# Kernel tuning notes

Hardware: AMD Instinct MI355X
Metric: run time of the kernel (lower is better)

## Reference

```python
import jax, jax.numpy as jnp
import numpy as np

B, S, H = 2, 2048, 2048
NH = 16
HD = H // NH          # 128
ROT = HD // 4         # rotary_dim = head_dim * 0.25 = 32
VP = 320              # v_proj_dim
BASE = 10000.0


def setup_inputs() -> dict:
    key = jax.random.key(0)
    ks = jax.random.split(key, 10)
    sc = lambda fan_in: 1.0 / np.sqrt(fan_in)
    return {
        "hidden_states": jax.random.normal(ks[0], (B, S, H), jnp.float32),
        "Wqkv": jax.random.normal(ks[1], (3 * H, H), jnp.float32) * sc(H),
        "bqkv": jnp.zeros((3 * H,), jnp.float32),
        "Wc": jax.random.normal(ks[2], (VP, H), jnp.float32) * sc(H),
        "bc": jnp.zeros((VP,), jnp.float32),
        "Wr": jax.random.normal(ks[3], (H, VP), jnp.float32) * sc(VP),
        "br": jnp.zeros((H,), jnp.float32),
        "Wd": jax.random.normal(ks[4], (H, H), jnp.float32) * sc(H),
        "bd": jnp.zeros((H,), jnp.float32),
    }


def _rope_tables(seq_len, rot_dim, dtype):
    inv_freq = 1.0 / (BASE ** (jnp.arange(0, rot_dim, 2, dtype=jnp.float32) / rot_dim))
    t = jnp.arange(seq_len, dtype=jnp.float32)
    freqs = jnp.outer(t, inv_freq)                      # [S, rot/2]
    emb = jnp.concatenate([freqs, freqs], axis=-1)      # [S, rot]
    return jnp.cos(emb).astype(dtype), jnp.sin(emb).astype(dtype)


def _rotate_half(x):
    x1, x2 = jnp.split(x, 2, axis=-1)
    return jnp.concatenate([-x2, x1], axis=-1)


def reference(hidden_states, Wqkv, bqkv, Wc, bc, Wr, br, Wd, bd):
    b, s, h = hidden_states.shape
    qkv = hidden_states @ Wqkv.T + bqkv                 # [B,S,3H]
    qkv = qkv.reshape(b, s, 3, NH, HD)
    qkv = jnp.transpose(qkv, (2, 0, 3, 1, 4))           # [3,B,NH,S,HD]
    q, k, v = qkv[0], qkv[1], qkv[2]

    cos, sin = _rope_tables(s, ROT, hidden_states.dtype)  # [S,ROT]
    cos = cos[None, None, :, :]
    sin = sin[None, None, :, :]
    q_rot, q_pass = q[..., :ROT], q[..., ROT:]
    k_rot, k_pass = k[..., :ROT], k[..., ROT:]
    q_rot = q_rot * cos + _rotate_half(q_rot) * sin
    k_rot = k_rot * cos + _rotate_half(k_rot) * sin
    q = jnp.concatenate([q_rot, q_pass], axis=-1)
    k = jnp.concatenate([k_rot, k_pass], axis=-1)

    # V low-rank compress / restore
    v_hidden = jnp.transpose(v, (0, 2, 1, 3)).reshape(b, s, h)  # [B,S,H]
    v_restored = (v_hidden @ Wc.T + bc) @ Wr.T + br             # [B,S,H]
    v_heads = jnp.transpose(v_restored.reshape(b, s, NH, HD), (0, 2, 1, 3))  # [B,NH,S,HD]

    scale = HD ** -0.5
    scores = jnp.einsum('bhqd,bhkd->bhqk', q, k) * scale
    causal = jnp.triu(jnp.full((s, s), -jnp.inf, scores.dtype), k=1)
    scores = scores + causal
    attn = jax.nn.softmax(scores, axis=-1)
    out = jnp.einsum('bhqk,bhkd->bhqd', attn, v_heads)
    out = jnp.transpose(out, (0, 2, 1, 3)).reshape(b, s, h)
    return out @ Wd.T + bd
```

## Files before the change

### kernel.cpp

```cpp
#include <hip/hip_runtime.h>

typedef unsigned short u16;
typedef unsigned int u32;
typedef __bf16 bf16x8 __attribute__((ext_vector_type(8)));
typedef float f32x4 __attribute__((ext_vector_type(4)));

#define BB 2
#define SS 2048
#define HH 2048
#define NHH 16
#define HDD 128

__device__ __forceinline__ float b2f(u16 u) {
  union { u32 i; float f; } v; v.i = ((u32)u) << 16; return v.f;
}
__device__ __forceinline__ u16 f2b(float f) {
  union { float f; u32 i; } v; v.f = f;
  u32 x = v.i;
  u32 r = (x + 0x7fffu + ((x >> 16) & 1u)) >> 16;
  return (u16)r;
}

__device__ __forceinline__ void gload_lds16(const u16* g, u16* l) {
  __builtin_amdgcn_global_load_lds(
      (const __attribute__((address_space(1))) u32*)g,
      (__attribute__((address_space(3))) u32*)l, 16, 0, 0);
}

__global__ __launch_bounds__(256) void cvt_kernel(
    const float* __restrict__ s0, u16* __restrict__ d0, int n0,
    const float* __restrict__ s1, u16* __restrict__ d1, int n1,
    const float* __restrict__ s2, u16* __restrict__ d2, int n2,
    const float* __restrict__ s3, u16* __restrict__ d3, int n3,
    const float* __restrict__ s4, u16* __restrict__ d4, int n4)
{
  const float* s; u16* d; int n;
  switch (blockIdx.y) {
    case 0: s = s0; d = d0; n = n0; break;
    case 1: s = s1; d = d1; n = n1; break;
    case 2: s = s2; d = d2; n = n2; break;
    case 3: s = s3; d = d3; n = n3; break;
    default: s = s4; d = d4; n = n4; break;
  }
  int nq = n >> 2;
  for (int q = blockIdx.x * 256 + threadIdx.x; q < nq; q += gridDim.x * 256) {
    float4 v = *(const float4*)(s + (size_t)q * 4);
    ushort4 o;
    o.x = f2b(v.x); o.y = f2b(v.y); o.z = f2b(v.z); o.w = f2b(v.w);
    *(ushort4*)(d + (size_t)q * 4) = o;
  }
}


template<int ISA>
__device__ __forceinline__ void stage_half(
    const u16* __restrict__ src, u16* ldsmat, int h,
    int tb, int kb, int ld, int wid, int lane)
{
#pragma unroll
  for (int l = 0; l < 2; ++l) {
    const int i = wid * 2 + l;
    const int rp = i * 8 + (lane >> 3);
    int r;
    if (ISA) r = (rp & 63) + ((rp >> 6) << 7) + h * 64;
    else     r = ((rp >> 5) << 6) + h * 32 + (rp & 31);
    const int c = (lane & 7) ^ (lane >> 3);
    gload_lds16(src + (size_t)(tb + r) * ld + kb + c * 8,
                ldsmat + (size_t)(h * 128 + i * 8) * 64);
  }
}

#define BAR()   __builtin_amdgcn_s_barrier()
#define PRIO1() __builtin_amdgcn_s_setprio(1)
#define PRIO0() __builtin_amdgcn_s_setprio(0)

#define LDA_READ(BP, MH) do {                                                  \
  const u16* _p = (BP);                                                        \
  _Pragma("unroll") for (int mi = 0; mi < 4; ++mi) {                           \
    const int _rho = (MH) * 128 + wr * 64 + mi * 16 + lm;                      \
    _Pragma("unroll") for (int ks = 0; ks < 2; ++ks)                           \
      af[mi][ks] = *(const bf16x8*)&_p[(size_t)_rho * 64 +                     \
                                       ((((ks << 2) + quad) ^ (lm & 7)) << 3)];\
  }                                                                            \
} while (0)

#define LDB_READ(BP, NH) do {                                                  \
  const u16* _p = (BP);                                                        \
  _Pragma("unroll") for (int ni = 0; ni < 2; ++ni) {                           \
    const int _rho = (NH) * 128 + wc * 32 + ni * 16 + lm;                      \
    _Pragma("unroll") for (int ks = 0; ks < 2; ++ks)                           \
      bfr[NH][ni][ks] = *(const bf16x8*)&_p[(size_t)_rho * 64 +                \
                                       ((((ks << 2) + quad) ^ (lm & 7)) << 3)];\
  }                                                                            \
} while (0)

#define MFMA_Q(MH, NH) do {                                                    \
  _Pragma("unroll") for (int mi = 0; mi < 4; ++mi)                             \
    _Pragma("unroll") for (int ni = 0; ni < 2; ++ni)                           \
      _Pragma("unroll") for (int ks = 0; ks < 2; ++ks)                         \
        acc[(MH) * 4 + mi][(NH) * 2 + ni] =                                    \
            __builtin_amdgcn_mfma_f32_16x16x32_bf16(                           \
                af[mi][ks], bfr[NH][ni][ks],                                   \
                acc[(MH) * 4 + mi][(NH) * 2 + ni], 0, 0, 0);                   \
} while (0)

__global__ __launch_bounds__(512, 2) void gemm256_rope_kernel(
    const u16* __restrict__ A, const u16* __restrict__ Bw,
    const float* __restrict__ bias, u16* __restrict__ C,
    int M, int N, int K, int lda, int ldb, int ldc)
{
  __shared__ u16 lds[2][2][256 * 64];
  const int t = threadIdx.x;
  const int lane = t & 63, wid = t >> 6;
  const int wr = wid >> 2, wc = wid & 3;
  const int quad = lane >> 4, lm = lane & 15;

  const int nwg = gridDim.x * gridDim.y;
  const int lid = blockIdx.y * gridDim.x + blockIdx.x;
  const int sb = (lid & 7) * (nwg >> 3) + (lid >> 3);
  const int m0 = (sb % gridDim.y) * 256, n0 = (sb / gridDim.y) * 256;

  u16* As0 = &lds[0][0][0]; u16* Bs0 = &lds[0][1][0];
  u16* As1 = &lds[1][0][0]; u16* Bs1 = &lds[1][1][0];

  f32x4 acc[8][4] = {};
  bf16x8 af[4][2];
  bf16x8 bfr[2][2][2];

  const int NT = K >> 6;

  stage_half<1>(A,  As0, 0, m0, 0, lda, wid, lane);
  stage_half<0>(Bw, Bs0, 0, n0, 0, ldb, wid, lane);
  stage_half<0>(Bw, Bs0, 1, n0, 0, ldb, wid, lane);
  stage_half<1>(A,  As0, 1, m0, 0, lda, wid, lane);
  asm volatile("s_waitcnt vmcnt(4)" ::: "memory");
  stage_half<1>(A,  As1, 0, m0, 64, lda, wid, lane);
  stage_half<0>(Bw, Bs1, 0, n0, 64, ldb, wid, lane);
  stage_half<0>(Bw, Bs1, 1, n0, 64, ldb, wid, lane);
  asm volatile("s_waitcnt vmcnt(6)" ::: "memory");
  BAR();

  for (int it2 = 0; it2 < (NT >> 1); ++it2) {
    int kb1 = (it2 * 2 + 1) << 6;
    int kb2 = (it2 * 2 + 2) << 6; if (kb2 >= K) kb2 -= K;
    int kb3 = (it2 * 2 + 3) << 6; if (kb3 >= K) kb3 -= K;

    LDA_READ(As0, 0); LDB_READ(Bs0, 0);
    stage_half<1>(A, As1, 1, m0, kb1, lda, wid, lane);
    BAR(); PRIO1(); MFMA_Q(0, 0); PRIO0(); BAR();
    LDB_READ(Bs0, 1);
    stage_half<1>(A, As0, 0, m0, kb2, lda, wid, lane);
    BAR(); PRIO1(); MFMA_Q(0, 1); PRIO0(); BAR();
    LDA_READ(As0, 1);
    stage_half<0>(Bw, Bs0, 0, n0, kb2, ldb, wid, lane);
    BAR(); PRIO1(); MFMA_Q(1, 1); PRIO0(); BAR();
    stage_half<0>(Bw, Bs0, 1, n0, kb2, ldb, wid, lane);
    asm volatile("s_waitcnt vmcnt(6)" ::: "memory");
    BAR(); PRIO1(); MFMA_Q(1, 0); PRIO0(); BAR();
    LDA_READ(As1, 0); LDB_READ(Bs1, 0);
    stage_half<1>(A, As0, 1, m0, kb2, lda, wid, lane);
    BAR(); PRIO1(); MFMA_Q(0, 0); PRIO0(); BAR();
    LDB_READ(Bs1, 1);
    stage_half<1>(A, As1, 0, m0, kb3, lda, wid, lane);
    BAR(); PRIO1(); MFMA_Q(0, 1); PRIO0(); BAR();
    LDA_READ(As1, 1);
    stage_half<0>(Bw, Bs1, 0, n0, kb3, ldb, wid, lane);
    BAR(); PRIO1(); MFMA_Q(1, 1); PRIO0(); BAR();
    stage_half<0>(Bw, Bs1, 1, n0, kb3, ldb, wid, lane);
    asm volatile("s_waitcnt vmcnt(6)" ::: "memory");
    BAR(); PRIO1(); MFMA_Q(1, 0); PRIO0(); BAR();
  }
  asm volatile("s_waitcnt vmcnt(0)" ::: "memory");

  const int cbase = n0 + wc * 64;
  const float ropefreq = exp2f(-(float)lm * 0.8304820237218406f);
  const bool do_rope = ((wc & 1) == 0) && (cbase < 4096);
  float b0 = 0.f, b1 = 0.f;
  if (do_rope) { b0 = bias[cbase + lm]; b1 = bias[cbase + lm + 16]; }

#pragma unroll
  for (int mi8 = 0; mi8 < 8; ++mi8) {
    const int gm = m0 + wr * 128 + mi8 * 16 + quad * 4;
    int jstart = 0;
    if (do_rope) {
      jstart = 2;
      const int gn0 = cbase + lm, gn1 = gn0 + 16;
#pragma unroll
      for (int rg = 0; rg < 4; ++rg) {
        int rs = gm + rg;
        float sn, cs;
        __sincosf((float)(rs & (SS - 1)) * ropefreq, &sn, &cs);
        float x0 = acc[mi8][0][rg] + b0, x1 = acc[mi8][1][rg] + b1;
        C[(size_t)rs * ldc + gn0] = f2b(x0 * cs - x1 * sn);
        C[(size_t)rs * ldc + gn1] = f2b(x1 * cs + x0 * sn);
      }
    }
#pragma unroll
    for (int nj = 0; nj < 4; ++nj) {
      if (nj < jstart) continue;
      const int gn = cbase + nj * 16 + lm;
      if (gn < N) {
        f32x4 a = acc[mi8][nj];
        float bs = bias[gn];
#pragma unroll
        for (int rg = 0; rg < 4; ++rg)
          C[(size_t)(gm + rg) * ldc + gn] = f2b(a[rg] + bs);
      }
    }
  }
}

template<int OUT_F32, int ROPE, int BIAS_ROW>
__global__ __launch_bounds__(256) void gemm_bias_kernel(
    const u16* __restrict__ A, const u16* __restrict__ Bw,
    const float* __restrict__ bias, void* __restrict__ Cv,
    int M, int N, int K, int lda, int ldb, int ldc,
    size_t strideB, size_t strideC)
{
  __shared__ u16 Asf[128 * 4 * 8];
  __shared__ u16 Bsf[128 * 4 * 8];
  const int t = threadIdx.x;
  const int m0 = blockIdx.y * 128;
  const int n0 = blockIdx.x * 128;
  const int lane = t & 63, wid = t >> 6;
  const int wm = (wid >> 1) * 64, wn = (wid & 1) * 64;
  const int quad = lane >> 4, lm = lane & 15;

  const u16* Bz = Bw + (size_t)blockIdx.z * strideB;

  const int r16 = lane >> 2;
  const int swz = ((lane >> 2) & 3) ^ ((lane >> 4) & 3);
  const int kc = ((lane & 3) ^ swz) * 8;
  const int fswz = (lm & 3) ^ ((lm >> 2) & 3);

  f32x4 acc[4][4] = {};

  for (int k0 = 0; k0 < K; k0 += 32) {
    __syncthreads();
#pragma unroll
    for (int it = 0; it < 2; ++it) {
      int g = wid * 2 + it;
      int r = g * 16 + r16;
      gload_lds16(A + (size_t)(m0 + r) * lda + k0 + kc, &Asf[(size_t)g * 512]);
      gload_lds16(Bz + (size_t)(n0 + r) * ldb + k0 + kc, &Bsf[(size_t)g * 512]);
    }
    __syncthreads();
    bf16x8 af[4], bf[4];
#pragma unroll
    for (int i = 0; i < 4; ++i) {
      int row = wm + i * 16 + lm;
      af[i] = *(const bf16x8*)&Asf[(size_t)(row * 4 + (quad ^ fswz)) * 8];
    }
#pragma unroll
    for (int j = 0; j < 4; ++j) {
      int row = wn + j * 16 + lm;
      bf[j] = *(const bf16x8*)&Bsf[(size_t)(row * 4 + (quad ^ fswz)) * 8];
    }
#pragma unroll
    for (int i = 0; i < 4; ++i)
#pragma unroll
      for (int j = 0; j < 4; ++j)
        acc[i][j] = __builtin_amdgcn_mfma_f32_16x16x32_bf16(af[i], bf[j], acc[i][j], 0, 0, 0);
  }

  float* Cf = (float*)Cv + (OUT_F32 ? (size_t)blockIdx.z * strideC : 0);
  u16* Cu = (u16*)Cv + (OUT_F32 ? 0 : (size_t)blockIdx.z * strideC);
  const float ropefreq = ROPE ? exp2f(-(float)lm * 0.8304820237218406f) : 0.f;
  const bool do_rope = ROPE && (wn == 0) && (n0 < 4096);

#pragma unroll
  for (int i = 0; i < 4; ++i) {
    int gm = m0 + wm + i * 16 + quad * 4;
    int jstart = 0;
    if (do_rope) {
      jstart = 2;
      int gn0 = n0 + lm, gn1 = gn0 + 16;
      float b0 = bias[gn0], b1 = bias[gn1];
#pragma unroll
      for (int rg = 0; rg < 4; ++rg) {
        int rs = gm + rg;
        float sn, cs;
        __sincosf((float)(rs & (SS - 1)) * ropefreq, &sn, &cs);
        float x0 = acc[i][0][rg] + b0, x1 = acc[i][1][rg] + b1;
        Cu[(size_t)rs * ldc + gn0] = f2b(x0 * cs - x1 * sn);
        Cu[(size_t)rs * ldc + gn1] = f2b(x1 * cs + x0 * sn);
      }
    }
#pragma unroll
    for (int j = 0; j < 4; ++j) {
      if (j < jstart) continue;
      int gn = n0 + wn + j * 16 + lm;
      if (gn < N) {
        f32x4 a = acc[i][j];
#pragma unroll
        for (int rg = 0; rg < 4; ++rg) {
          float bsv = BIAS_ROW ? bias[gm + rg] : bias[gn];
          if (OUT_F32) Cf[(size_t)(gm + rg) * ldc + gn] = a[rg] + bsv;
          else         Cu[(size_t)(gm + rg) * ldc + gn] = f2b(a[rg] + bsv);
        }
      }
    }
  }
}

__global__ __launch_bounds__(256) void attn_mfma_kernel(
    const u16* __restrict__ qkv, const u16* __restrict__ vrt, u16* __restrict__ out)
{
  __shared__ u16 Kt[64 * 16 * 8];
  __shared__ u16 Vt[8][128][8];
  __shared__ u16 Pa[4][16 * 64];

  const int t = threadIdx.x;
  const int lane = t & 63, w = t >> 6;
  const int quad = lane >> 4, lm = lane & 15;
  const int lid = blockIdx.x;
  const int sbx = (lid & 7) * 64 + (lid >> 3);
  const int bh = sbx >> 4;
  const int pr = sbx & 15;
  const int b = bh >> 4, h = bh & 15;

  const float scale = 0.08838834764831845f;
  const u16* kbase = qkv + (size_t)b * SS * 6144 + 2048 + h * 128;
  const u16* vbase = vrt + (size_t)bh * 128 * 2048;
  u16* pw = &Pa[w][0];

#pragma unroll 1
  for (int ps = 0; ps < 2; ++ps) {
    const int qt = ps ? pr : (31 - pr);
    const int qw = qt * 64 + w * 16;
    const int nkt = qt + 1;

    bf16x8 qf[4];
    {
      const u16* qsrc = qkv + (size_t)(b * SS + qw + lm) * 6144 + h * 128 + quad * 8;
#pragma unroll
      for (int dc = 0; dc < 4; ++dc) qf[dc] = *(const bf16x8*)(qsrc + dc * 32);
    }

    f32x4 Oa[8] = {};
    float m_i = -1e30f, l_i = 0.f;

#pragma unroll 1
    for (int kt = 0; kt < nkt; ++kt) {
      const int kb = kt * 64;
      __syncthreads();
#pragma unroll
      for (int it = 0; it < 4; ++it) {
        int c = t + it * 256;
        int kp = c >> 4, dq = c & 15;
        *(uint4*)&Kt[(size_t)(kp * 16 + (dq ^ (kp & 15))) * 8] =
            *(const uint4*)(kbase + (size_t)(kb + kp) * 6144 + dq * 8);
        int d = c >> 3, kq = c & 7;
        *(uint4*)&Vt[kq][d][0] =
            *(const uint4*)(vbase + (size_t)d * 2048 + kb + kq * 8);
      }
      __syncthreads();

      f32x4 sa[4] = {};
#pragma unroll
      for (int ct = 0; ct < 4; ++ct) {
#pragma unroll
        for (int dc = 0; dc < 4; ++dc) {
          bf16x8 kf = *(const bf16x8*)&Kt[(size_t)((ct * 16 + lm) * 16 +
                                                   ((dc * 4 + quad) ^ lm)) * 8];
          sa[ct] = __builtin_amdgcn_mfma_f32_16x16x32_bf16(kf, qf[dc], sa[ct], 0, 0, 0);
        }
      }
#pragma unroll
      for (int ct = 0; ct < 4; ++ct)
#pragma unroll
        for (int r = 0; r < 4; ++r) sa[ct][r] *= scale;

      if (kt == nkt - 1) {
        int qpos = qw + lm;
#pragma unroll
        for (int ct = 0; ct < 4; ++ct) {
#pragma unroll
          for (int r = 0; r < 4; ++r)
            if (kb + ct * 16 + quad * 4 + r > qpos) sa[ct][r] = -1e30f;
        }
      }

      float mx = sa[0][0];
#pragma unroll
      for (int ct = 0; ct < 4; ++ct)
#pragma unroll
        for (int r = 0; r < 4; ++r) mx = fmaxf(mx, sa[ct][r]);
      mx = fmaxf(mx, __shfl_xor(mx, 16, 64));
      mx = fmaxf(mx, __shfl_xor(mx, 32, 64));
      float mnew = fmaxf(m_i, mx);
      float alpha = __expf(m_i - mnew);
      float ssum = 0.f;
#pragma unroll
      for (int ct = 0; ct < 4; ++ct)
#pragma unroll
        for (int r = 0; r < 4; ++r) {
          float p = __expf(sa[ct][r] - mnew);
          sa[ct][r] = p;
          ssum += p;
        }
      ssum += __shfl_xor(ssum, 16, 64);
      ssum += __shfl_xor(ssum, 32, 64);
      l_i = l_i * alpha + ssum;
      m_i = mnew;

      float ar[4];
#pragma unroll
      for (int r = 0; r < 4; ++r) ar[r] = __shfl(alpha, quad * 4 + r, 64);
#pragma unroll
      for (int dt = 0; dt < 8; ++dt)
#pragma unroll
        for (int r = 0; r < 4; ++r) Oa[dt][r] *= ar[r];

#pragma unroll
      for (int ct = 0; ct < 4; ++ct) {
        uint2 pk;
        pk.x = (u32)f2b(sa[ct][0]) | ((u32)f2b(sa[ct][1]) << 16);
        pk.y = (u32)f2b(sa[ct][2]) | ((u32)f2b(sa[ct][3]) << 16);
        int u = ct * 2 + (quad >> 1);
        *(uint2*)(pw + lm * 64 + ((u ^ (lm & 7)) * 8) + (quad & 1) * 4) = pk;
      }
      bf16x8 pf0 = *(const bf16x8*)(pw + lm * 64 + ((quad ^ (lm & 7)) * 8));
      bf16x8 pf1 = *(const bf16x8*)(pw + lm * 64 + (((4 + quad) ^ (lm & 7)) * 8));

#pragma unroll
      for (int dt = 0; dt < 8; ++dt) {
        bf16x8 vf0 = *(const bf16x8*)&Vt[quad][dt * 16 + lm][0];
        bf16x8 vf1 = *(const bf16x8*)&Vt[4 + quad][dt * 16 + lm][0];
        Oa[dt] = __builtin_amdgcn_mfma_f32_16x16x32_bf16(pf0, vf0, Oa[dt], 0, 0, 0);
        Oa[dt] = __builtin_amdgcn_mfma_f32_16x16x32_bf16(pf1, vf1, Oa[dt], 0, 0, 0);
      }
    }

    float inv = 1.0f / l_i;
    float ir[4];
#pragma unroll
    for (int r = 0; r < 4; ++r) ir[r] = __shfl(inv, quad * 4 + r, 64);
    u16* dst = out + (size_t)(b * SS + qw + quad * 4) * 2048 + h * 128 + lm;
#pragma unroll
    for (int r = 0; r < 4; ++r)
#pragma unroll
      for (int dt = 0; dt < 8; ++dt)
        dst[(size_t)r * 2048 + dt * 16] = f2b(Oa[dt][r] * ir[r]);
  }
}

extern "C" void kernel_launch(void* const* d_in, const int* in_sizes, int n_in,
                              void* d_out, int out_size, void* d_ws, size_t ws_size,
                              hipStream_t stream)
{
  (void)in_sizes; (void)n_in; (void)out_size; (void)ws_size;
  const float* X    = (const float*)d_in[0];
  const float* Wqkv = (const float*)d_in[1];
  const float* bqkv = (const float*)d_in[2];
  const float* Wc   = (const float*)d_in[3];
  const float* bc   = (const float*)d_in[4];
  const float* Wr   = (const float*)d_in[5];
  const float* br   = (const float*)d_in[6];
  const float* Wd   = (const float*)d_in[7];
  const float* bd   = (const float*)d_in[8];
  float* out = (float*)d_out;

  char* ws = (char*)d_ws;
  u16* QKV   = (u16*)(ws);
  u16* Xb    = (u16*)(ws + 50331648);
  u16* AO    = (u16*)(ws + 50331648);
  u16* Wqkvb = (u16*)(ws + 67108864);
  u16* VrT   = (u16*)(ws + 67108864);
  u16* Wcb   = (u16*)(ws + 92274688);
  u16* Wrb   = (u16*)(ws + 93585408);
  u16* Cb    = (u16*)(ws + 94896128);
  u16* Wdb   = (u16*)(ws + 97517568);

  dim3 blk(256);

  cvt_kernel<<<dim3(512, 5), blk, 0, stream>>>(
      X, Xb, 4096 * 2048,
      Wqkv, Wqkvb, 6144 * 2048,
      Wc, Wcb, 320 * 2048,
      Wr, Wrb, 2048 * 320,
      Wd, Wdb, 2048 * 2048);

  gemm256_rope_kernel<<<dim3(24, 16), dim3(512), 0, stream>>>(
      Xb, Wqkvb, bqkv, QKV, 4096, 6144, 2048, 2048, 2048, 6144);
  gemm_bias_kernel<0, 0, 0><<<dim3(3, 32), blk, 0, stream>>>(
      QKV + 4096, Wcb, bc, Cb, 4096, 320, 2048, 6144, 2048, 320, 0, 0);
  gemm_bias_kernel<0, 0, 1><<<dim3(16, 16, 2), blk, 0, stream>>>(
      Wrb, Cb, br, VrT, 2048, 2048, 320, 320, 320, 2048,
      (size_t)2048 * 320, (size_t)4194304);
  attn_mfma_kernel<<<dim3(512), blk, 0, stream>>>(QKV, VrT, AO);
  gemm_bias_kernel<1, 0, 0><<<dim3(16, 32), blk, 0, stream>>>(
      AO, Wdb, bd, out, 4096, 2048, 2048, 2048, 2048, 2048, 0, 0);
}
```

Before: 484.8 us.

## Fold V projection into compress weight to skip computing V activations

Precomputes the product of the compress weight with the V slice of Wqkv (plus a folded bias) so the compressed V comes straight from X with a K=2048, N=320 GEMM. The QKV GEMM then only produces Q and K (N=4096 instead of 6144). This drops roughly a third of the big projection's FLOPs in exchange for a small weight-weight GEMM, a transpose kernel and a bias kernel that run on every call. The extra rounding of the fused weight to bf16 slightly changes numerics.

```diff
diff --git a/kernel.cpp b/kernel.cpp
--- a/kernel.cpp
+++ b/kernel.cpp
@@ -49,6 +49,50 @@
     o.x = f2b(v.x); o.y = f2b(v.y); o.z = f2b(v.z); o.w = f2b(v.w);
     *(ushort4*)(d + (size_t)q * 4) = o;
   }
+}
+
+__global__ __launch_bounds__(256) void transpose_wv_kernel(
+    const float* __restrict__ Wqkv, u16* __restrict__ WvT)
+{
+  __shared__ float tile[64][65];
+  const int t = threadIdx.x;
+  const int r0 = blockIdx.y * 64;
+  const int c0 = blockIdx.x * 64;
+  const int tr = t >> 4;
+  const int tc = (t & 15) * 4;
+#pragma unroll
+  for (int i = 0; i < 4; ++i) {
+    int r = tr + i * 16;
+    float4 v = *(const float4*)(Wqkv + (size_t)(4096 + r0 + r) * 2048 + c0 + tc);
+    tile[r][tc] = v.x; tile[r][tc + 1] = v.y; tile[r][tc + 2] = v.z; tile[r][tc + 3] = v.w;
+  }
+  __syncthreads();
+#pragma unroll
+  for (int i = 0; i < 4; ++i) {
+    int n = tr + i * 16;
+    ushort4 o;
+    o.x = f2b(tile[tc + 0][n]);
+    o.y = f2b(tile[tc + 1][n]);
+    o.z = f2b(tile[tc + 2][n]);
+    o.w = f2b(tile[tc + 3][n]);
+    *(ushort4*)(WvT + (size_t)(c0 + n) * 2048 + r0 + tc) = o;
+  }
+}
+
+__global__ __launch_bounds__(256) void bc2_kernel(
+    const u16* __restrict__ Wcb, const float* __restrict__ bqkv,
+    const float* __restrict__ bc, float* __restrict__ bc2)
+{
+  const int t = threadIdx.x;
+  const int lane = t & 63, w = t >> 6;
+  const int row = blockIdx.x * 4 + w;
+  const float* bv = bqkv + 4096;
+  float s = 0.f;
+  for (int j = lane; j < 2048; j += 64)
+    s += b2f(Wcb[(size_t)row * 2048 + j]) * bv[j];
+#pragma unroll
+  for (int o = 32; o; o >>= 1) s += __shfl_xor(s, o, 64);
+  if (lane == 0) bc2[row] = bc[row] + s;
 }
 
 
@@ -210,7 +254,7 @@
   }
 }
 
-template<int OUT_F32, int ROPE, int BIAS_ROW>
+template<int OUT_F32, int ROPE, int BIAS_ROW, int NOBIAS>
 __global__ __launch_bounds__(256) void gemm_bias_kernel(
     const u16* __restrict__ A, const u16* __restrict__ Bw,
     const float* __restrict__ bias, void* __restrict__ Cv,
@@ -294,7 +338,7 @@
         f32x4 a = acc[i][j];
 #pragma unroll
         for (int rg = 0; rg < 4; ++rg) {
-          float bsv = BIAS_ROW ? bias[gm + rg] : bias[gn];
+          float bsv = NOBIAS ? 0.f : (BIAS_ROW ? bias[gm + rg] : bias[gn]);
           if (OUT_F32) Cf[(size_t)(gm + rg) * ldc + gn] = a[rg] + bsv;
           else         Cu[(size_t)(gm + rg) * ldc + gn] = f2b(a[rg] + bsv);
         }
@@ -471,6 +515,9 @@
   u16* Wrb   = (u16*)(ws + 93585408);
   u16* Cb    = (u16*)(ws + 94896128);
   u16* Wdb   = (u16*)(ws + 97517568);
+  u16* WvTb  = (u16*)(ws + 105906176);
+  u16* Wvc   = (u16*)(ws + 114294784);
+  float* bc2 = (float*)(ws + 115867648);
 
   dim3 blk(256);
 
@@ -481,14 +528,19 @@
       Wr, Wrb, 2048 * 320,
       Wd, Wdb, 2048 * 2048);
 
-  gemm256_rope_kernel<<<dim3(24, 16), dim3(512), 0, stream>>>(
-      Xb, Wqkvb, bqkv, QKV, 4096, 6144, 2048, 2048, 2048, 6144);
-  gemm_bias_kernel<0, 0, 0><<<dim3(3, 32), blk, 0, stream>>>(
-      QKV + 4096, Wcb, bc, Cb, 4096, 320, 2048, 6144, 2048, 320, 0, 0);
-  gemm_bias_kernel<0, 0, 1><<<dim3(16, 16, 2), blk, 0, stream>>>(
+  transpose_wv_kernel<<<dim3(32, 32), blk, 0, stream>>>(Wqkv, WvTb);
+  bc2_kernel<<<dim3(80), blk, 0, stream>>>(Wcb, bqkv, bc, bc2);
+  gemm_bias_kernel<0, 0, 0, 1><<<dim3(16, 3), blk, 0, stream>>>(
+      Wcb, WvTb, bc, Wvc, 320, 2048, 2048, 2048, 2048, 2048, 0, 0);
+
+  gemm256_rope_kernel<<<dim3(16, 16), dim3(512), 0, stream>>>(
+      Xb, Wqkvb, bqkv, QKV, 4096, 4096, 2048, 2048, 2048, 6144);
+  gemm_bias_kernel<0, 0, 0, 0><<<dim3(3, 32), blk, 0, stream>>>(
+      Xb, Wvc, bc2, Cb, 4096, 320, 2048, 2048, 2048, 320, 0, 0);
+  gemm_bias_kernel<0, 0, 1, 0><<<dim3(16, 16, 2), blk, 0, stream>>>(
       Wrb, Cb, br, VrT, 2048, 2048, 320, 320, 320, 2048,
       (size_t)2048 * 320, (size_t)4194304);
   attn_mfma_kernel<<<dim3(512), blk, 0, stream>>>(QKV, VrT, AO);
-  gemm_bias_kernel<1, 0, 0><<<dim3(16, 32), blk, 0, stream>>>(
+  gemm_bias_kernel<1, 0, 0, 0><<<dim3(16, 32), blk, 0, stream>>>(
       AO, Wdb, bd, out, 4096, 2048, 2048, 2048, 2048, 2048, 0, 0);
 }
```

New measurement: 489.8 us. About the same (+1.0%).
